# Kernel tuning notes

Measured on AMD Instinct MI355X. Metric: run time of the kernel, lower is better.

The kernel has to match this reference:

```python
import jax, jax.numpy as jnp
import numpy as np

BN_EPS = 1e-5


def three_nn(unknown, known):
    # unknown: (B,n,3), known: (B,m,3) -> dist (B,n,3), idx (B,n,3)
    d2 = (jnp.sum(unknown**2, -1)[:, :, None]
          + jnp.sum(known**2, -1)[:, None, :]
          - 2.0 * jnp.einsum('bnd,bmd->bnm', unknown, known))
    neg_d2, idx = jax.lax.top_k(-d2, 3)  # 3 smallest squared distances
    dist = jnp.sqrt(jnp.maximum(-neg_d2, 0.0))
    return dist, idx


def three_interpolate(points, idx, weight):
    # points: (B,m,c), idx: (B,n,3), weight: (B,n,3) -> (B,n,c)
    gathered = jax.vmap(lambda f, i: f[i])(points, idx)  # (B,n,3,c)
    return jnp.einsum('bnk,bnkc->bnc', weight, gathered)


def conv_bn_relu(x, W, b, g, beta):
    # 1x1 conv over points == per-point linear; BN over (batch, points)
    y = jnp.einsum('bnc,oc->bno', x, W) + b
    mu = jnp.mean(y, axis=(0, 1))
    var = jnp.var(y, axis=(0, 1))
    y = (y - mu) * jax.lax.rsqrt(var + BN_EPS) * g + beta
    return jax.nn.relu(y)


def setup_inputs() -> dict:
    key = jax.random.key(0)
    ks = jax.random.split(key, 8)
    B, n, m, C1, C2 = 8, 8192, 2048, 128, 256
    Cin = C1 + C2  # 384
    H = 256
    return {
        'unknown': jax.random.normal(ks[0], (B, n, 3), jnp.float32),
        'known': jax.random.normal(ks[1], (B, m, 3), jnp.float32),
        'unknow_feats': jax.random.normal(ks[2], (B, n, C1), jnp.float32),
        'known_feats': jax.random.normal(ks[3], (B, m, C2), jnp.float32),
        'W1': jax.random.normal(ks[4], (H, Cin), jnp.float32) * (1.0 / np.sqrt(Cin)),
        'b1': jnp.zeros((H,), jnp.float32),
        'g1': jnp.ones((H,), jnp.float32),
        'beta1': jnp.zeros((H,), jnp.float32),
        'W2': jax.random.normal(ks[5], (H, H), jnp.float32) * (1.0 / np.sqrt(H)),
        'b2': jnp.zeros((H,), jnp.float32),
        'g2': jnp.ones((H,), jnp.float32),
        'beta2': jnp.zeros((H,), jnp.float32),
    }


def reference(unknown, known, unknow_feats, known_feats,
              W1, b1, g1, beta1, W2, b2, g2, beta2):
    dist, idx = three_nn(unknown, known)
    dist = dist + 1e-10
    dist_recip = 1.0 / dist
    weight = dist_recip / jnp.sum(dist_recip, axis=2, keepdims=True)  # (B,n,3)
    interpolated = three_interpolate(known_feats, idx, weight)        # (B,n,C2)
    new_points = jnp.concatenate([interpolated, unknow_feats], axis=-1)  # (B,n,C1+C2)
    new_points = conv_bn_relu(new_points, W1, b1, g1, beta1)
    new_points = conv_bn_relu(new_points, W2, b2, g2, beta2)
    return new_points  # (B,n,mlp[-1])
```

## Files before the change

### kernel.cpp

```cpp
#include <hip/hip_runtime.h>

#define BQ   8
#define NQ   8192
#define MK   2048
#define C1v  128
#define C2v  256
#define CIN  384
#define HH   256
#define MTOT (BQ*NQ)

#define NCHUNK 8
#define CHSZ   (MK/NCHUNK)

typedef __attribute__((ext_vector_type(8))) __bf16 bf16x8;
typedef __attribute__((ext_vector_type(4))) float f32x4;
typedef __attribute__((ext_vector_type(8))) unsigned short us8;
typedef __attribute__((ext_vector_type(4))) unsigned short us4;
typedef __attribute__((ext_vector_type(2))) unsigned short us2;

__device__ __forceinline__ unsigned short f2bf(float f) {
  unsigned int u = __builtin_bit_cast(unsigned int, f);
  u += 0x7fffu + ((u >> 16) & 1u);
  return (unsigned short)(u >> 16);
}
__device__ __forceinline__ float bf2f(unsigned short h) {
  unsigned int u = ((unsigned int)h) << 16;
  return __builtin_bit_cast(float, u);
}

__device__ __forceinline__ void gload16(const void* g, void* l) {
  __builtin_amdgcn_global_load_lds((const __attribute__((address_space(1))) void*)g,
                                   (__attribute__((address_space(3))) void*)l, 16, 0, 0);
}

#define SCORE(k4) (fmaf((k4).x, ux, fmaf((k4).y, uy, (k4).z * uz)) + (k4).w)

__device__ __forceinline__ double packsd(float s, int negj) {
  unsigned long long u = __builtin_bit_cast(unsigned long long, (double)s)
                       | (unsigned long long)(unsigned int)negj;
  return __builtin_bit_cast(double, u);
}

#define INS3D(s0, s1, s2, t)                                  \
  do {                                                        \
    double _hi0 = fmax(s0, (t)), _lo0 = fmin(s0, (t));        \
    double _hi1 = fmax(s1, _lo0), _lo1 = fmin(s1, _lo0);      \
    s0 = _hi0; s1 = _hi1; s2 = fmax(s2, _lo1);                \
  } while (0)

__global__ __launch_bounds__(256)
void prep_kernel(const float* __restrict__ W1, const float* __restrict__ W2,
                 const float* __restrict__ known,
                 unsigned short* __restrict__ w1b, unsigned short* __restrict__ w2b,
                 float* __restrict__ stats, float4* __restrict__ kprep) {
  int i = blockIdx.x * 256 + threadIdx.x;
  if (i < HH*CIN) w1b[i] = f2bf(W1[i]);
  else if (i < HH*CIN + HH*HH) w2b[i - HH*CIN] = f2bf(W2[i - HH*CIN]);
  int z = i - (HH*CIN + HH*HH);
  if (z >= 0 && z < 1024) stats[z] = 0.f;
  int z2 = i - (HH*CIN + HH*HH + 1024);
  if (z2 >= 0 && z2 < BQ*MK) {
    const float* kp = known + (size_t)z2 * 3;
    float x = kp[0], y = kp[1], zz = kp[2];
    kprep[z2] = make_float4(x, y, zz, -0.5f*(x*x + y*y + zz*zz));
  }
}

__global__ __launch_bounds__(512)
void nn_kernel(const float* __restrict__ unknown, const float4* __restrict__ kprep,
               int* __restrict__ widx, float* __restrict__ wwgt) {
  __shared__ double pd[NCHUNK][64][3];
  const int b = blockIdx.y;
  const int tid = threadIdx.x;
  const int wave = tid >> 6, lane = tid & 63;

  const int q = blockIdx.x * 64 + lane;
  const float* up = unknown + ((size_t)b * NQ + q) * 3;
  const float ux = up[0], uy = up[1], uz = up[2];
  const float nu = ux*ux + uy*uy + uz*uz;
  const int jbase = wave * CHSZ;
  const float4* cp = kprep + (b << 11) + __builtin_amdgcn_readfirstlane(jbase);

  double A0=-1e300, A1=-1e300, A2=-1e300;
  double B0=-1e300, B1=-1e300, B2=-1e300;
  #pragma unroll 4
  for (int j = 0; j < CHSZ; j += 2) {
    float4 ka = cp[j];
    float4 kc = cp[j+1];
    float sA = SCORE(ka);
    float sB = SCORE(kc);
    double da = packsd(sA, 2047 - (jbase + j));
    double db = packsd(sB, 2047 - (jbase + j + 1));
    INS3D(A0, A1, A2, da);
    INS3D(B0, B1, B2, db);
  }
  INS3D(A0, A1, A2, B0);
  INS3D(A0, A1, A2, B1);
  INS3D(A0, A1, A2, B2);
  pd[wave][lane][0] = A0; pd[wave][lane][1] = A1; pd[wave][lane][2] = A2;
  __syncthreads();

  if (tid < 64) {
    double f0=-1e300, f1=-1e300, f2=-1e300;
    #pragma unroll
    for (int c = 0; c < NCHUNK; ++c) {
      INS3D(f0, f1, f2, pd[c][tid][0]);
      INS3D(f0, f1, f2, pd[c][tid][1]);
      INS3D(f0, f1, f2, pd[c][tid][2]);
    }
    unsigned long long u0 = __builtin_bit_cast(unsigned long long, f0);
    unsigned long long u1 = __builtin_bit_cast(unsigned long long, f1);
    unsigned long long u2 = __builtin_bit_cast(unsigned long long, f2);
    int x0 = 2047 - (int)(u0 & 2047ULL);
    int x1 = 2047 - (int)(u1 & 2047ULL);
    int x2 = 2047 - (int)(u2 & 2047ULL);
    float s0 = (float)__builtin_bit_cast(double, u0 & ~2047ULL);
    float s1 = (float)__builtin_bit_cast(double, u1 & ~2047ULL);
    float s2 = (float)__builtin_bit_cast(double, u2 & ~2047ULL);
    float d0 = sqrtf(fmaxf(nu - 2.f*s0, 0.f)) + 1e-10f;
    float d1 = sqrtf(fmaxf(nu - 2.f*s1, 0.f)) + 1e-10f;
    float d2 = sqrtf(fmaxf(nu - 2.f*s2, 0.f)) + 1e-10f;
    float r0 = 1.f/d0, r1 = 1.f/d1, r2 = 1.f/d2;
    float rs = 1.f/(r0 + r1 + r2);
    size_t p = (size_t)b * NQ + q;
    widx[p*3+0] = x0;    widx[p*3+1] = x1;    widx[p*3+2] = x2;
    wwgt[p*3+0] = r0*rs; wwgt[p*3+1] = r1*rs; wwgt[p*3+2] = r2*rs;
  }
}

__global__ __launch_bounds__(256)
void interp_kernel(const float* __restrict__ kf, const float* __restrict__ uf,
                   const int* __restrict__ widx, const float* __restrict__ wwgt,
                   unsigned short* __restrict__ X) {
  const int p = blockIdx.x * 4 + (threadIdx.x >> 6);
  const int lane = threadIdx.x & 63;
  const int b = p >> 13, q = p & 8191;
  const int*   ip = widx + (size_t)p * 3;
  const float* wp = wwgt + (size_t)p * 3;
  int   j0 = ip[0], j1 = ip[1], j2 = ip[2];
  float w0 = wp[0], w1 = wp[1], w2 = wp[2];
  const float4* f0 = (const float4*)(kf + ((size_t)b*MK + j0) * C2v);
  const float4* f1 = (const float4*)(kf + ((size_t)b*MK + j1) * C2v);
  const float4* f2 = (const float4*)(kf + ((size_t)b*MK + j2) * C2v);
  float4 a = f0[lane], c = f1[lane], d = f2[lane];
  unsigned short* xr = X + (size_t)p * CIN;
  us4 v;
  v[0] = f2bf(w0*a.x + w1*c.x + w2*d.x);
  v[1] = f2bf(w0*a.y + w1*c.y + w2*d.y);
  v[2] = f2bf(w0*a.z + w1*c.z + w2*d.z);
  v[3] = f2bf(w0*a.w + w1*c.w + w2*d.w);
  *(us4*)(xr + lane*4) = v;
  float2 uu = *(const float2*)(uf + ((size_t)b*NQ + q) * C1v + lane*2);
  us2 w; w[0] = f2bf(uu.x); w[1] = f2bf(uu.y);
  *(us2*)(xr + C2v + lane*2) = w;
}

__global__ __launch_bounds__(256)
void gemm_kernel(const unsigned short* __restrict__ A,
                 const unsigned short* __restrict__ Bw,
                 const float* __restrict__ bias,
                 unsigned short* __restrict__ Out,
                 float* __restrict__ gsum, float* __restrict__ gsq) {
  constexpr int K = CIN;
  __shared__ unsigned short As[128][64];
  __shared__ unsigned short Bs[128][64];
  const int tid  = threadIdx.x;
  const int lane = tid & 63;
  const int wave = tid >> 6;
  const int wid  = blockIdx.x;
  const int slot = wid & 15;
  const int bm = ((wid >> 4) << 3) | (slot & 7);
  const int bn = slot >> 3;
  const int wm = wave >> 1, wn = wave & 1;

  f32x4 acc[4][4];
  const f32x4 zero = {0.f, 0.f, 0.f, 0.f};
  #pragma unroll
  for (int m = 0; m < 4; ++m)
    #pragma unroll
    for (int n = 0; n < 4; ++n) acc[m][n] = zero;

  for (int k0 = 0; k0 < K; k0 += 64) {
    #pragma unroll
    for (int i = 0; i < 4; ++i) {
      const int cbase = wave*64 + i*256;
      const int c = cbase + lane;
      const int row = c >> 3, col = (c & 7) * 8;
      gload16(Bw + ((size_t)(bn*128 + row))*K + k0 + col, (unsigned short*)Bs + cbase*8);
      gload16(A  + ((size_t)(bm*128 + row))*K + k0 + col, (unsigned short*)As + cbase*8);
    }
    __syncthreads();
    const int kq = (lane >> 4) * 8;
    #pragma unroll
    for (int kk = 0; kk < 64; kk += 32) {
      bf16x8 af[4], bfr[4];
      #pragma unroll
      for (int m = 0; m < 4; ++m)
        af[m] = *(const bf16x8*)&As[wm*64 + m*16 + (lane & 15)][kk + kq];
      #pragma unroll
      for (int n = 0; n < 4; ++n)
        bfr[n] = *(const bf16x8*)&Bs[wn*64 + n*16 + (lane & 15)][kk + kq];
      #pragma unroll
      for (int m = 0; m < 4; ++m)
        #pragma unroll
        for (int n = 0; n < 4; ++n)
          acc[m][n] = __builtin_amdgcn_mfma_f32_16x16x32_bf16(af[m], bfr[n], acc[m][n], 0, 0, 0);
    }
    __syncthreads();
  }

  float* s_sum = (float*)&As[0][0];
  float* s_sq  = s_sum + 256;
  #pragma unroll
  for (int n = 0; n < 4; ++n) {
    const int cb   = wn*64 + n*16 + (lane & 15);
    const int gcol = bn*128 + cb;
    const float bv = bias[gcol];
    float sum = 0.f, sq = 0.f;
    #pragma unroll
    for (int m = 0; m < 4; ++m) {
      const size_t grow = (size_t)bm*128 + wm*64 + m*16 + (lane >> 4)*4;
      #pragma unroll
      for (int qq = 0; qq < 4; ++qq) {
        float y = acc[m][n][qq] + bv;
        sum += y; sq += y*y;
        Out[(grow+qq)*256 + gcol] = f2bf(y);
      }
    }
    sum += __shfl_xor(sum, 16, 64); sum += __shfl_xor(sum, 32, 64);
    sq  += __shfl_xor(sq , 16, 64); sq  += __shfl_xor(sq , 32, 64);
    if (lane < 16) { s_sum[wm*128 + cb] = sum; s_sq[wm*128 + cb] = sq; }
  }
  __syncthreads();
  if (tid < 128) {
    atomicAdd(&gsum[bn*128 + tid], s_sum[tid] + s_sum[128 + tid]);
    atomicAdd(&gsq [bn*128 + tid], s_sq [tid] + s_sq [128 + tid]);
  }
}

__global__ __launch_bounds__(256)
void gemm2_kernel(const unsigned short* __restrict__ A,
                  const unsigned short* __restrict__ Bw,
                  const float* __restrict__ bias,
                  unsigned short* __restrict__ Out,
                  float* __restrict__ gsum, float* __restrict__ gsq,
                  const float* __restrict__ gsum1, const float* __restrict__ gsq1,
                  const float* __restrict__ g1, const float* __restrict__ be1) {
  constexpr int K = HH;
  __shared__ unsigned short As[128][64];
  __shared__ unsigned short Bs[128][64];
  __shared__ float sc_l[HH], sh_l[HH];
  const int tid  = threadIdx.x;
  const int lane = tid & 63;
  const int wave = tid >> 6;
  const int wid  = blockIdx.x;
  const int slot = wid & 15;
  const int bm = ((wid >> 4) << 3) | (slot & 7);
  const int bn = slot >> 3;
  const int wm = wave >> 1, wn = wave & 1;

  {
    float mu  = gsum1[tid] * (1.f/65536.f);
    float var = gsq1[tid]  * (1.f/65536.f) - mu*mu;
    float sc  = g1[tid] * rsqrtf(var + 1e-5f);
    sc_l[tid] = sc;
    sh_l[tid] = be1[tid] - mu*sc;
  }
  __syncthreads();

  f32x4 acc[4][4];
  const f32x4 zero = {0.f, 0.f, 0.f, 0.f};
  #pragma unroll
  for (int m = 0; m < 4; ++m)
    #pragma unroll
    for (int n = 0; n < 4; ++n) acc[m][n] = zero;

  for (int k0 = 0; k0 < K; k0 += 64) {
    #pragma unroll
    for (int i = 0; i < 4; ++i) {
      const int cbase = wave*64 + i*256;
      const int c = cbase + lane;
      const int row = c >> 3, col = (c & 7) * 8;
      gload16(Bw + ((size_t)(bn*128 + row))*K + k0 + col, (unsigned short*)Bs + cbase*8);
      us8 v = *(const us8*)(A + ((size_t)(bm*128 + row))*K + k0 + col);
      us8 o;
      #pragma unroll
      for (int j = 0; j < 8; ++j) {
        float y = fmaxf(fmaf(bf2f(v[j]), sc_l[k0+col+j], sh_l[k0+col+j]), 0.f);
        o[j] = f2bf(y);
      }
      *(us8*)((unsigned short*)As + cbase*8 + lane*8) = o;
    }
    __syncthreads();
    const int kq = (lane >> 4) * 8;
    #pragma unroll
    for (int kk = 0; kk < 64; kk += 32) {
      bf16x8 af[4], bfr[4];
      #pragma unroll
      for (int m = 0; m < 4; ++m)
        af[m] = *(const bf16x8*)&As[wm*64 + m*16 + (lane & 15)][kk + kq];
      #pragma unroll
      for (int n = 0; n < 4; ++n)
        bfr[n] = *(const bf16x8*)&Bs[wn*64 + n*16 + (lane & 15)][kk + kq];
      #pragma unroll
      for (int m = 0; m < 4; ++m)
        #pragma unroll
        for (int n = 0; n < 4; ++n)
          acc[m][n] = __builtin_amdgcn_mfma_f32_16x16x32_bf16(af[m], bfr[n], acc[m][n], 0, 0, 0);
    }
    __syncthreads();
  }

  float* s_sum = (float*)&As[0][0];
  float* s_sq  = s_sum + 256;
  #pragma unroll
  for (int n = 0; n < 4; ++n) {
    const int cb   = wn*64 + n*16 + (lane & 15);
    const int gcol = bn*128 + cb;
    const float bv = bias[gcol];
    float sum = 0.f, sq = 0.f;
    #pragma unroll
    for (int m = 0; m < 4; ++m) {
      const size_t grow = (size_t)bm*128 + wm*64 + m*16 + (lane >> 4)*4;
      #pragma unroll
      for (int qq = 0; qq < 4; ++qq) {
        float y = acc[m][n][qq] + bv;
        sum += y; sq += y*y;
        Out[(grow+qq)*256 + gcol] = f2bf(y);
      }
    }
    sum += __shfl_xor(sum, 16, 64); sum += __shfl_xor(sum, 32, 64);
    sq  += __shfl_xor(sq , 16, 64); sq  += __shfl_xor(sq , 32, 64);
    if (lane < 16) { s_sum[wm*128 + cb] = sum; s_sq[wm*128 + cb] = sq; }
  }
  __syncthreads();
  if (tid < 128) {
    atomicAdd(&gsum[bn*128 + tid], s_sum[tid] + s_sum[128 + tid]);
    atomicAdd(&gsq [bn*128 + tid], s_sq [tid] + s_sq [128 + tid]);
  }
}

__global__ __launch_bounds__(256)
void final_kernel(const unsigned short* __restrict__ Y2, float* __restrict__ Out,
                  const float* __restrict__ gsum, const float* __restrict__ gsq,
                  const float* __restrict__ g2, const float* __restrict__ be2) {
  __shared__ float sc[256], sh[256];
  {
    float mu  = gsum[threadIdx.x] * (1.f/65536.f);
    float var = gsq[threadIdx.x]  * (1.f/65536.f) - mu*mu;
    float scv = g2[threadIdx.x] * rsqrtf(var + 1e-5f);
    sc[threadIdx.x] = scv;
    sh[threadIdx.x] = be2[threadIdx.x] - mu*scv;
  }
  __syncthreads();
  size_t i = ((size_t)blockIdx.x * 256 + threadIdx.x) * 8;
  int c0 = (int)(i & 255);
  us8 v = *(const us8*)(Y2 + i);
  float4 o1, o2;
  o1.x = fmaxf(fmaf(bf2f(v[0]), sc[c0+0], sh[c0+0]), 0.f);
  o1.y = fmaxf(fmaf(bf2f(v[1]), sc[c0+1], sh[c0+1]), 0.f);
  o1.z = fmaxf(fmaf(bf2f(v[2]), sc[c0+2], sh[c0+2]), 0.f);
  o1.w = fmaxf(fmaf(bf2f(v[3]), sc[c0+3], sh[c0+3]), 0.f);
  o2.x = fmaxf(fmaf(bf2f(v[4]), sc[c0+4], sh[c0+4]), 0.f);
  o2.y = fmaxf(fmaf(bf2f(v[5]), sc[c0+5], sh[c0+5]), 0.f);
  o2.z = fmaxf(fmaf(bf2f(v[6]), sc[c0+6], sh[c0+6]), 0.f);
  o2.w = fmaxf(fmaf(bf2f(v[7]), sc[c0+7], sh[c0+7]), 0.f);
  *(float4*)(Out + i)     = o1;
  *(float4*)(Out + i + 4) = o2;
}

extern "C" void kernel_launch(void* const* d_in, const int* in_sizes, int n_in,
                              void* d_out, int out_size, void* d_ws, size_t ws_size,
                              hipStream_t stream) {
  const float* unknown = (const float*)d_in[0];
  const float* known   = (const float*)d_in[1];
  const float* uf      = (const float*)d_in[2];
  const float* kf      = (const float*)d_in[3];
  const float* W1      = (const float*)d_in[4];
  const float* b1      = (const float*)d_in[5];
  const float* g1      = (const float*)d_in[6];
  const float* be1     = (const float*)d_in[7];
  const float* W2      = (const float*)d_in[8];
  const float* b2      = (const float*)d_in[9];
  const float* g2      = (const float*)d_in[10];
  const float* be2     = (const float*)d_in[11];

  char* ws = (char*)d_ws;
  unsigned short* X    = (unsigned short*)(ws);
  unsigned short* Y1   = (unsigned short*)(ws + 50331648);
  unsigned short* w1b  = (unsigned short*)(ws + 83886080);
  unsigned short* w2b  = (unsigned short*)(ws + 84082688);
  int*            widx = (int*)  (ws + 84213760);
  float*          wwgt = (float*)(ws + 85000192);
  float*          stats= (float*)(ws + 85786624);
  float4*         kprep= (float4*)(ws + 85794816);
  float *sum1 = stats,        *sq1 = stats + 256;
  float *sum2 = stats + 512,  *sq2 = stats + 768;
  float* out = (float*)d_out;

  prep_kernel<<<708, 256, 0, stream>>>(W1, W2, known, w1b, w2b, stats, kprep);
  nn_kernel<<<dim3(128, 8), 512, 0, stream>>>(unknown, kprep, widx, wwgt);
  interp_kernel<<<16384, 256, 0, stream>>>(kf, uf, widx, wwgt, X);
  gemm_kernel<<<1024, 256, 0, stream>>>(X, w1b, b1, Y1, sum1, sq1);
  gemm2_kernel<<<1024, 256, 0, stream>>>(Y1, w2b, b2, X, sum2, sq2, sum1, sq1, g1, be1);
  final_kernel<<<8192, 256, 0, stream>>>(X, out, sum2, sq2, g2, be2);
}
```

Before: 173.0 us.

## Fuse three-point interpolation and concat into GEMM1 A-tile loading

```diff
diff --git a/kernel.cpp b/kernel.cpp
--- a/kernel.cpp
+++ b/kernel.cpp
@@ -31,6 +31,12 @@
 __device__ __forceinline__ void gload16(const void* g, void* l) {
   __builtin_amdgcn_global_load_lds((const __attribute__((address_space(1))) void*)g,
                                    (__attribute__((address_space(3))) void*)l, 16, 0, 0);
+}
+
+__device__ __forceinline__ unsigned int cvtpk_bf16(float lo, float hi) {
+  unsigned int r;
+  asm("v_cvt_pk_bf16_f32 %0, %1, %2" : "=v"(r) : "v"(lo), "v"(hi));
+  return r;
 }
 
 #define SCORE(k4) (fmaf((k4).x, ux, fmaf((k4).y, uy, (k4).z * uz)) + (k4).w)
@@ -129,34 +135,8 @@
 }
 
 __global__ __launch_bounds__(256)
-void interp_kernel(const float* __restrict__ kf, const float* __restrict__ uf,
-                   const int* __restrict__ widx, const float* __restrict__ wwgt,
-                   unsigned short* __restrict__ X) {
-  const int p = blockIdx.x * 4 + (threadIdx.x >> 6);
-  const int lane = threadIdx.x & 63;
-  const int b = p >> 13, q = p & 8191;
-  const int*   ip = widx + (size_t)p * 3;
-  const float* wp = wwgt + (size_t)p * 3;
-  int   j0 = ip[0], j1 = ip[1], j2 = ip[2];
-  float w0 = wp[0], w1 = wp[1], w2 = wp[2];
-  const float4* f0 = (const float4*)(kf + ((size_t)b*MK + j0) * C2v);
-  const float4* f1 = (const float4*)(kf + ((size_t)b*MK + j1) * C2v);
-  const float4* f2 = (const float4*)(kf + ((size_t)b*MK + j2) * C2v);
-  float4 a = f0[lane], c = f1[lane], d = f2[lane];
-  unsigned short* xr = X + (size_t)p * CIN;
-  us4 v;
-  v[0] = f2bf(w0*a.x + w1*c.x + w2*d.x);
-  v[1] = f2bf(w0*a.y + w1*c.y + w2*d.y);
-  v[2] = f2bf(w0*a.z + w1*c.z + w2*d.z);
-  v[3] = f2bf(w0*a.w + w1*c.w + w2*d.w);
-  *(us4*)(xr + lane*4) = v;
-  float2 uu = *(const float2*)(uf + ((size_t)b*NQ + q) * C1v + lane*2);
-  us2 w; w[0] = f2bf(uu.x); w[1] = f2bf(uu.y);
-  *(us2*)(xr + C2v + lane*2) = w;
-}
-
-__global__ __launch_bounds__(256)
-void gemm_kernel(const unsigned short* __restrict__ A,
+void gemm1_fused(const float* __restrict__ kf, const float* __restrict__ uf,
+                 const int* __restrict__ widx, const float* __restrict__ wwgt,
                  const unsigned short* __restrict__ Bw,
                  const float* __restrict__ bias,
                  unsigned short* __restrict__ Out,
@@ -173,6 +153,21 @@
   const int bn = slot >> 3;
   const int wm = wave >> 1, wn = wave & 1;
 
+  unsigned int vo0[4], vo1[4], vo2[4], voU[4];
+  float w0r[4], w1r[4], w2r[4];
+  #pragma unroll
+  for (int i = 0; i < 4; ++i) {
+    const int c = wave*64 + i*256 + lane;
+    const int row = c >> 3, colB = (c & 7) * 32;
+    const int p = bm*128 + row;
+    const int b = p >> 13;
+    w0r[i] = wwgt[p*3+0]; w1r[i] = wwgt[p*3+1]; w2r[i] = wwgt[p*3+2];
+    vo0[i] = ((unsigned)((b << 11) + widx[p*3+0]) << 10) + colB;
+    vo1[i] = ((unsigned)((b << 11) + widx[p*3+1]) << 10) + colB;
+    vo2[i] = ((unsigned)((b << 11) + widx[p*3+2]) << 10) + colB;
+    voU[i] = (unsigned)p * 512u + colB;
+  }
+
   f32x4 acc[4][4];
   const f32x4 zero = {0.f, 0.f, 0.f, 0.f};
   #pragma unroll
@@ -180,14 +175,45 @@
     #pragma unroll
     for (int n = 0; n < 4; ++n) acc[m][n] = zero;
 
-  for (int k0 = 0; k0 < K; k0 += 64) {
+  const char* kfb = (const char*)kf;
+  const char* ufb = (const char*)uf;
+
+  #pragma unroll
+  for (int t = 0; t < 6; ++t) {
+    const int k0 = t * 64;
     #pragma unroll
     for (int i = 0; i < 4; ++i) {
       const int cbase = wave*64 + i*256;
       const int c = cbase + lane;
-      const int row = c >> 3, col = (c & 7) * 8;
-      gload16(Bw + ((size_t)(bn*128 + row))*K + k0 + col, (unsigned short*)Bs + cbase*8);
-      gload16(A  + ((size_t)(bm*128 + row))*K + k0 + col, (unsigned short*)As + cbase*8);
+      const int brow = c >> 3, bcol = (c & 7) * 8;
+      gload16(Bw + ((size_t)(bn*128 + brow))*K + k0 + bcol, (unsigned short*)Bs + cbase*8);
+      float4 r0, r1;
+      if (t < 4) {
+        float4 a0 = *(const float4*)(kfb + vo0[i] + k0*4);
+        float4 a1 = *(const float4*)(kfb + vo0[i] + k0*4 + 16);
+        float4 e0 = *(const float4*)(kfb + vo1[i] + k0*4);
+        float4 e1 = *(const float4*)(kfb + vo1[i] + k0*4 + 16);
+        float4 g0 = *(const float4*)(kfb + vo2[i] + k0*4);
+        float4 g1 = *(const float4*)(kfb + vo2[i] + k0*4 + 16);
+        const float w0 = w0r[i], w1 = w1r[i], w2 = w2r[i];
+        r0.x = w0*a0.x + w1*e0.x + w2*g0.x;
+        r0.y = w0*a0.y + w1*e0.y + w2*g0.y;
+        r0.z = w0*a0.z + w1*e0.z + w2*g0.z;
+        r0.w = w0*a0.w + w1*e0.w + w2*g0.w;
+        r1.x = w0*a1.x + w1*e1.x + w2*g1.x;
+        r1.y = w0*a1.y + w1*e1.y + w2*g1.y;
+        r1.z = w0*a1.z + w1*e1.z + w2*g1.z;
+        r1.w = w0*a1.w + w1*e1.w + w2*g1.w;
+      } else {
+        r0 = *(const float4*)(ufb + voU[i] + (k0 - 256)*4);
+        r1 = *(const float4*)(ufb + voU[i] + (k0 - 256)*4 + 16);
+      }
+      uint4 ov;
+      ov.x = cvtpk_bf16(r0.x, r0.y);
+      ov.y = cvtpk_bf16(r0.z, r0.w);
+      ov.z = cvtpk_bf16(r1.x, r1.y);
+      ov.w = cvtpk_bf16(r1.z, r1.w);
+      *(uint4*)((unsigned short*)As + (size_t)c*8) = ov;
     }
     __syncthreads();
     const int kq = (lane >> 4) * 8;
@@ -400,8 +426,7 @@
 
   prep_kernel<<<708, 256, 0, stream>>>(W1, W2, known, w1b, w2b, stats, kprep);
   nn_kernel<<<dim3(128, 8), 512, 0, stream>>>(unknown, kprep, widx, wwgt);
-  interp_kernel<<<16384, 256, 0, stream>>>(kf, uf, widx, wwgt, X);
-  gemm_kernel<<<1024, 256, 0, stream>>>(X, w1b, b1, Y1, sum1, sq1);
+  gemm1_fused<<<1024, 256, 0, stream>>>(kf, uf, widx, wwgt, w1b, b1, Y1, sum1, sq1);
   gemm2_kernel<<<1024, 256, 0, stream>>>(Y1, w2b, b2, X, sum2, sq2, sum1, sq1, g1, be1);
   final_kernel<<<8192, 256, 0, stream>>>(X, out, sum2, sq2, g2, be2);
 }
```

Result: faster. 163.3 us (-5.6%).
